# Performance work log

Hardware: AMD Instinct MI355X
Metric: run time of the kernel (lower is better)

Reference implementation:

```python
import jax, jax.numpy as jnp
import numpy as np
from jax import lax

VOCAB, EMB, HID = 50257, 256, 256
B, T = 64, 2048

def setup_inputs() -> dict:
    key = jax.random.key(0)
    ks = jax.random.split(key, 6)
    s = 1.0 / np.sqrt(HID)
    return {
        "sequence": jax.random.randint(ks[0], (B, T), 0, VOCAB),
        "embedding": jax.random.normal(ks[1], (VOCAB, EMB), jnp.float32),
        "w_ih": jax.random.uniform(ks[2], (3 * HID, EMB), jnp.float32, -s, s),
        "w_hh": jax.random.uniform(ks[3], (3 * HID, HID), jnp.float32, -s, s),
        "b_ih": jax.random.uniform(ks[4], (3 * HID,), jnp.float32, -s, s),
        "b_hh": jax.random.uniform(ks[5], (3 * HID,), jnp.float32, -s, s),
    }

def reference(sequence, embedding, w_ih, w_hh, b_ih, b_hh):
    # sequence: [B,T] int tokens. Original loops per-timestep; math == one GRU pass.
    H = w_hh.shape[1]
    x = embedding[sequence]                       # [B,T,E]
    x = jnp.transpose(x, (1, 0, 2))               # [T,B,E] (time-major)
    # input-side gate pre-activations for all steps at once: [T,B,3H]
    gi = jnp.einsum('tbe,ge->tbg', x, w_ih) + b_ih

    def step(h, gi_t):
        gh = h @ w_hh.T + b_hh                    # [B,3H]
        i_r, i_z, i_n = jnp.split(gi_t, 3, axis=-1)
        h_r, h_z, h_n = jnp.split(gh, 3, axis=-1)
        r = jax.nn.sigmoid(i_r + h_r)
        z = jax.nn.sigmoid(i_z + h_z)
        n = jnp.tanh(i_n + r * h_n)
        h_new = (1.0 - z) * n + z * h
        return h_new, None

    h0 = jnp.zeros((sequence.shape[0], H), dtype=embedding.dtype)
    hT, _ = lax.scan(step, h0, gi)
    return hT[None]                                # [1,B,H] like torch GRU hidden
```

## Files before the change

### kernel.cpp

```cpp
#include <hip/hip_runtime.h>
#include <hip/hip_fp16.h>

#define TSEQ   2048
#define NB     64
#define NE     256
#define NH     256
#define NG     768
#define TCH    64
#define NCHUNK (TSEQ / TCH)

using half2_t = __attribute__((ext_vector_type(2))) _Float16;
typedef unsigned int u32x4 __attribute__((ext_vector_type(4)));
union U4 { u32x4 q; half2_t h[4]; };

__device__ __forceinline__ float dot2f(half2_t a, half2_t b, float c) {
#if __has_builtin(__builtin_amdgcn_fdot2)
  return __builtin_amdgcn_fdot2(a, b, c, false);
#else
  return c + (float)a[0] * (float)b[0] + (float)a[1] * (float)b[1];
#endif
}

__device__ __forceinline__ float fast_exp2(float x) {
#if __has_builtin(__builtin_amdgcn_exp2f)
  return __builtin_amdgcn_exp2f(x);
#else
  return exp2f(x);
#endif
}
__device__ __forceinline__ float fast_rcp(float x) {
#if __has_builtin(__builtin_amdgcn_rcpf)
  return __builtin_amdgcn_rcpf(x);
#else
  return 1.f / x;
#endif
}
__device__ __forceinline__ float sigm(float x) {
  return fast_rcp(1.f + fast_exp2(x * -1.44269504f));
}
__device__ __forceinline__ float tanh_fast(float x) {
  x = fminf(x, 15.f);
  float e = fast_exp2(x * 2.88539008f);
  return (e - 1.f) * fast_rcp(e + 1.f);
}

__global__ void prep_whh(const float* __restrict__ whh, unsigned int* __restrict__ w16) {
  int idx = blockIdx.x * 256 + threadIdx.x;
  if (idx >= 128 * NG) return;
  int row = idx % NG;
  int k2  = idx / NG;
  half2_t p;
  p[0] = (_Float16)whh[row * NH + 2 * k2];
  p[1] = (_Float16)whh[row * NH + 2 * k2 + 1];
  union { half2_t h; unsigned int u; } cvt;
  cvt.h = p;
  w16[(((k2 >> 2) * NG + row) << 2) | (k2 & 3)] = cvt.u;
}

__global__ __launch_bounds__(1024)
void fused_kernel(const int* __restrict__ seq, const float* __restrict__ emb,
                  const float* __restrict__ wih, const float* __restrict__ bih,
                  const float* __restrict__ bhh, const unsigned int* __restrict__ w16,
                  const float* __restrict__ rec_gi, float* __restrict__ gi_dst,
                  int gi_t0, float* __restrict__ h_state, float* __restrict__ out,
                  int rec_count, int chunk)
{
  __shared__ __align__(16) char smem[87552];
  const int tid = threadIdx.x;

  if ((int)blockIdx.x < rec_count) {
    _Float16* h16 = (_Float16*)smem;
    const int b    = blockIdx.x;
    const int lane = tid & 63;
    const int wv   = tid >> 6;
    const int j    = wv * 16 + (lane & 15);
    const int s    = lane >> 4;

#define LOADW(i)                                                              \
  u32x4 wr##i, wz##i, wn##i;                                                  \
  {                                                                           \
    const unsigned int* base = w16 + (((size_t)(s * 8 + (i)) * NG) << 2);     \
    wr##i = *(const u32x4*)(base + ((size_t)j << 2));                         \
    wz##i = *(const u32x4*)(base + ((size_t)(NH + j) << 2));                  \
    wn##i = *(const u32x4*)(base + ((size_t)(2 * NH + j) << 2));              \
  }
    LOADW(0) LOADW(1) LOADW(2) LOADW(3) LOADW(4) LOADW(5) LOADW(6) LOADW(7)
#undef LOADW
    asm volatile("" : "+v"(wr0), "+v"(wr1), "+v"(wr2), "+v"(wr3),
                      "+v"(wr4), "+v"(wr5), "+v"(wr6), "+v"(wr7));
    asm volatile("" : "+v"(wz0), "+v"(wz1), "+v"(wz2), "+v"(wz3),
                      "+v"(wz4), "+v"(wz5), "+v"(wz6), "+v"(wz7));
    asm volatile("" : "+v"(wn0), "+v"(wn1), "+v"(wn2), "+v"(wn3),
                      "+v"(wn4), "+v"(wn5), "+v"(wn6), "+v"(wn7));

    const float bn = bhh[2 * NH + j];
    float hreg = 0.f;
    if (chunk != 0) hreg = h_state[b * NH + j];
    if (s == 0) h16[j] = (_Float16)hreg;
    __syncthreads();

    const float* gpj = rec_gi + (size_t)b * NG + j;

#pragma unroll 1
    for (int t = 0; t < TCH; ++t) {
      const float gr = gpj[0], gz = gpj[NH], gn = gpj[2 * NH];

      float ar = 0.f, az = 0.f, an = 0.f;
      const char* hb = (const char*)h16 + ((t & 1) << 9) + (s << 7);

#define DOT(i)                                                                \
  {                                                                           \
    U4 hu; hu.q = *(const u32x4*)(hb + ((i) << 4));                           \
    U4 ru; ru.q = wr##i;                                                      \
    U4 zu; zu.q = wz##i;                                                      \
    U4 nu; nu.q = wn##i;                                                      \
    ar = dot2f(hu.h[0], ru.h[0], ar);                                         \
    az = dot2f(hu.h[0], zu.h[0], az);                                         \
    an = dot2f(hu.h[0], nu.h[0], an);                                         \
    ar = dot2f(hu.h[1], ru.h[1], ar);                                         \
    az = dot2f(hu.h[1], zu.h[1], az);                                         \
    an = dot2f(hu.h[1], nu.h[1], an);                                         \
    ar = dot2f(hu.h[2], ru.h[2], ar);                                         \
    az = dot2f(hu.h[2], zu.h[2], az);                                         \
    an = dot2f(hu.h[2], nu.h[2], an);                                         \
    ar = dot2f(hu.h[3], ru.h[3], ar);                                         \
    az = dot2f(hu.h[3], zu.h[3], az);                                         \
    an = dot2f(hu.h[3], nu.h[3], an);                                         \
  }
      DOT(0) DOT(1) DOT(2) DOT(3) DOT(4) DOT(5) DOT(6) DOT(7)
#undef DOT

      ar += __shfl_xor(ar, 16, 64);  ar += __shfl_xor(ar, 32, 64);
      az += __shfl_xor(az, 16, 64);  az += __shfl_xor(az, 32, 64);
      an += __shfl_xor(an, 16, 64);  an += __shfl_xor(an, 32, 64);

      const float r = sigm(gr + ar);
      const float z = sigm(gz + az);
      const float n = tanh_fast(gn + r * (an + bn));
      hreg = n + z * (hreg - n);

      if (s == 0) h16[(((t + 1) & 1) << 8) + j] = (_Float16)hreg;
      gpj += NB * NG;
      __syncthreads();
    }
    if (s == 0) {
      h_state[b * NH + j] = hreg;
      if (out) out[b * NH + j] = hreg;
    }
  } else {
    if (gi_dst == nullptr) return;
    float (*xs)[68]  = (float(*)[68])smem;
    float (*wsh)[68] = (float(*)[68])(smem + 17408);
    int*  tok        = (int*)(smem + 17408 + 69632);
    const int gb = blockIdx.x - rec_count;
    const int tl = gb & 63;
    const int g0 = (gb >> 6) * 256;
    const int t  = gi_t0 + tl;
    if (tid < 64) tok[tid] = seq[tid * TSEQ + t];
    const int tx = tid & 31;
    const int ty = tid >> 5;
    float acc[2][8];
#pragma unroll
    for (int i = 0; i < 2; ++i)
#pragma unroll
      for (int c8 = 0; c8 < 8; ++c8) acc[i][c8] = 0.f;

    for (int kb = 0; kb < 4; ++kb) {
      __syncthreads();
      {
        int r = tid >> 4, c = tid & 15;
        *(float4*)(&xs[r][c * 4]) =
            *(const float4*)(emb + (size_t)tok[r] * NE + kb * 64 + c * 4);
      }
#pragma unroll
      for (int it = 0; it < 4; ++it) {
        int i = it * 1024 + tid;
        int r = i >> 4, c = i & 15;
        *(float4*)(&wsh[r][c * 4]) =
            *(const float4*)(wih + (size_t)(g0 + r) * NE + kb * 64 + c * 4);
      }
      __syncthreads();
#pragma unroll 4
      for (int k4 = 0; k4 < 16; ++k4) {
        float4 xf[2], wf[8];
#pragma unroll
        for (int i = 0; i < 2; ++i) xf[i] = *(const float4*)(&xs[ty * 2 + i][k4 * 4]);
#pragma unroll
        for (int c8 = 0; c8 < 8; ++c8) wf[c8] = *(const float4*)(&wsh[tx + 32 * c8][k4 * 4]);
#pragma unroll
        for (int i = 0; i < 2; ++i)
#pragma unroll
          for (int c8 = 0; c8 < 8; ++c8)
            acc[i][c8] += xf[i].x * wf[c8].x + xf[i].y * wf[c8].y +
                          xf[i].z * wf[c8].z + xf[i].w * wf[c8].w;
      }
    }
#pragma unroll
    for (int i = 0; i < 2; ++i) {
      const int brow = ty * 2 + i;
      float* dst = gi_dst + ((size_t)(tl * NB + brow)) * NG + g0;
#pragma unroll
      for (int c8 = 0; c8 < 8; ++c8) {
        const int col = tx + 32 * c8;
        const int g = g0 + col;
        float bias = bih[g] + (g < 2 * NH ? bhh[g] : 0.f);
        dst[col] = acc[i][c8] + bias;
      }
    }
  }
}

extern "C" void kernel_launch(void* const* d_in, const int* in_sizes, int n_in,
                              void* d_out, int out_size, void* d_ws, size_t ws_size,
                              hipStream_t stream) {
  (void)in_sizes; (void)n_in; (void)out_size; (void)ws_size;
  const int*   seq = (const int*)d_in[0];
  const float* emb = (const float*)d_in[1];
  const float* wih = (const float*)d_in[2];
  const float* whh = (const float*)d_in[3];
  const float* bih = (const float*)d_in[4];
  const float* bhh = (const float*)d_in[5];
  float* out = (float*)d_out;
  char*  ws  = (char*)d_ws;

  unsigned int* w16     = (unsigned int*)(ws);
  float*        h_state = (float*)(ws + 393216);
  float*        gi0     = (float*)(ws + 458752);
  float*        gi1     = (float*)(ws + 458752 + 12582912);

  prep_whh<<<dim3(384), dim3(256), 0, stream>>>(whh, w16);

  fused_kernel<<<dim3(192), dim3(1024), 0, stream>>>(
      seq, emb, wih, bih, bhh, w16,
      nullptr, gi0, 0, h_state, nullptr, 0, 0);

  for (int c = 0; c < NCHUNK; ++c) {
    float* rd  = (c & 1) ? gi1 : gi0;
    float* wr_ = (c & 1) ? gi0 : gi1;
    const bool last = (c == NCHUNK - 1);
    const int grid  = last ? NB : NB + 192;
    fused_kernel<<<dim3(grid), dim3(1024), 0, stream>>>(
        seq, emb, wih, bih, bhh, w16,
        rd, last ? nullptr : wr_, (c + 1) * TCH, h_state,
        last ? out : nullptr, NB, c);
  }
}
```

Measured before the change: 2.674 ms.

## Move n-gate recurrent weights from registers into LDS and pad h buffer

The n-gate W_hh slice is repacked by a new prep kernel into a per-lane LDS image and loaded into shared memory at block start, so the recurrent loop keeps only the r and z weights in VGPRs. This cuts register pressure (32 fewer u32x4 registers per thread), which could allow better scheduling or avoid spills. The h double-buffer is also re-laid out with padded quarter strides to reduce LDS bank conflicts. The cost is an extra LDS read per dot step inside the serial loop and a larger shared allocation of about 129 KB.

```diff
diff --git a/kernel.cpp b/kernel.cpp
--- a/kernel.cpp
+++ b/kernel.cpp
@@ -8,6 +8,12 @@
 #define NG     768
 #define TCH    64
 #define NCHUNK (TSEQ / TCH)
+
+#define WN_BYTES   131072
+#define H_OFF      131072
+#define H_BUFSTR   576
+#define H_QSTR     144
+#define POOL_BYTES 132352
 
 using half2_t = __attribute__((ext_vector_type(2))) _Float16;
 typedef unsigned int u32x4 __attribute__((ext_vector_type(4)));
@@ -57,32 +63,62 @@
   w16[(((k2 >> 2) * NG + row) << 2) | (k2 & 3)] = cvt.u;
 }
 
+__global__ void prep_n(const float* __restrict__ whh, unsigned int* __restrict__ n_img) {
+  int idx32 = blockIdx.x * 256 + threadIdx.x;
+  if (idx32 >= 32768) return;
+  int idxh = idx32 * 2;
+  int wv   = idxh >> 12;
+  int r    = idxh & 4095;
+  int i    = r >> 9;
+  int r2   = r & 511;
+  int lane = r2 >> 3;
+  int e    = r2 & 7;
+  int j    = wv * 16 + (lane & 15);
+  int s    = lane >> 4;
+  int k    = s * 64 + i * 8 + e;
+  half2_t p;
+  p[0] = (_Float16)whh[(512 + j) * NH + k];
+  p[1] = (_Float16)whh[(512 + j) * NH + k + 1];
+  union { half2_t h; unsigned int u; } cvt;
+  cvt.h = p;
+  n_img[idx32] = cvt.u;
+}
+
 __global__ __launch_bounds__(1024)
 void fused_kernel(const int* __restrict__ seq, const float* __restrict__ emb,
                   const float* __restrict__ wih, const float* __restrict__ bih,
                   const float* __restrict__ bhh, const unsigned int* __restrict__ w16,
+                  const unsigned int* __restrict__ n_img,
                   const float* __restrict__ rec_gi, float* __restrict__ gi_dst,
                   int gi_t0, float* __restrict__ h_state, float* __restrict__ out,
                   int rec_count, int chunk)
 {
-  __shared__ __align__(16) char smem[87552];
+  __shared__ __align__(16) char smem[POOL_BYTES];
   const int tid = threadIdx.x;
 
   if ((int)blockIdx.x < rec_count) {
-    _Float16* h16 = (_Float16*)smem;
     const int b    = blockIdx.x;
     const int lane = tid & 63;
     const int wv   = tid >> 6;
     const int j    = wv * 16 + (lane & 15);
     const int s    = lane >> 4;
 
+    {
+      const char* nsrc = (const char*)n_img;
+      const int base = wv * 8192 + lane * 16;
+#pragma unroll
+      for (int it = 0; it < 8; ++it) {
+        *(u32x4*)(smem + base + it * 1024) =
+            *(const u32x4*)(nsrc + base + it * 1024);
+      }
+    }
+
 #define LOADW(i)                                                              \
-  u32x4 wr##i, wz##i, wn##i;                                                  \
+  u32x4 wr##i, wz##i;                                                         \
   {                                                                           \
     const unsigned int* base = w16 + (((size_t)(s * 8 + (i)) * NG) << 2);     \
     wr##i = *(const u32x4*)(base + ((size_t)j << 2));                         \
     wz##i = *(const u32x4*)(base + ((size_t)(NH + j) << 2));                  \
-    wn##i = *(const u32x4*)(base + ((size_t)(2 * NH + j) << 2));              \
   }
     LOADW(0) LOADW(1) LOADW(2) LOADW(3) LOADW(4) LOADW(5) LOADW(6) LOADW(7)
 #undef LOADW
@@ -90,30 +126,32 @@
                       "+v"(wr4), "+v"(wr5), "+v"(wr6), "+v"(wr7));
     asm volatile("" : "+v"(wz0), "+v"(wz1), "+v"(wz2), "+v"(wz3),
                       "+v"(wz4), "+v"(wz5), "+v"(wz6), "+v"(wz7));
-    asm volatile("" : "+v"(wn0), "+v"(wn1), "+v"(wn2), "+v"(wn3),
-                      "+v"(wn4), "+v"(wn5), "+v"(wn6), "+v"(wn7));
 
     const float bn = bhh[2 * NH + j];
     float hreg = 0.f;
     if (chunk != 0) hreg = h_state[b * NH + j];
-    if (s == 0) h16[j] = (_Float16)hreg;
+    if (s == 0) {
+      *(_Float16*)(smem + H_OFF + ((j >> 6) * H_QSTR) + ((j & 63) * 2)) =
+          (_Float16)hreg;
+    }
     __syncthreads();
 
     const float* gpj = rec_gi + (size_t)b * NG + j;
+    const char*  nb  = smem + wv * 8192 + lane * 16;
 
 #pragma unroll 1
     for (int t = 0; t < TCH; ++t) {
       const float gr = gpj[0], gz = gpj[NH], gn = gpj[2 * NH];
 
       float ar = 0.f, az = 0.f, an = 0.f;
-      const char* hb = (const char*)h16 + ((t & 1) << 9) + (s << 7);
+      const char* hb = smem + H_OFF + ((t & 1) ? H_BUFSTR : 0) + s * H_QSTR;
 
 #define DOT(i)                                                                \
   {                                                                           \
     U4 hu; hu.q = *(const u32x4*)(hb + ((i) << 4));                           \
+    U4 nu; nu.q = *(const u32x4*)(nb + ((i) << 10));                          \
     U4 ru; ru.q = wr##i;                                                      \
     U4 zu; zu.q = wz##i;                                                      \
-    U4 nu; nu.q = wn##i;                                                      \
     ar = dot2f(hu.h[0], ru.h[0], ar);                                         \
     az = dot2f(hu.h[0], zu.h[0], az);                                         \
     an = dot2f(hu.h[0], nu.h[0], an);                                         \
@@ -139,7 +177,10 @@
       const float n = tanh_fast(gn + r * (an + bn));
       hreg = n + z * (hreg - n);
 
-      if (s == 0) h16[(((t + 1) & 1) << 8) + j] = (_Float16)hreg;
+      if (s == 0) {
+        *(_Float16*)(smem + H_OFF + (((t + 1) & 1) ? H_BUFSTR : 0) +
+                     ((j >> 6) * H_QSTR) + ((j & 63) * 2)) = (_Float16)hreg;
+      }
       gpj += NB * NG;
       __syncthreads();
     }
@@ -224,14 +265,16 @@
   char*  ws  = (char*)d_ws;
 
   unsigned int* w16     = (unsigned int*)(ws);
-  float*        h_state = (float*)(ws + 393216);
-  float*        gi0     = (float*)(ws + 458752);
-  float*        gi1     = (float*)(ws + 458752 + 12582912);
+  unsigned int* n_img   = (unsigned int*)(ws + 393216);
+  float*        h_state = (float*)(ws + 524288);
+  float*        gi0     = (float*)(ws + 589824);
+  float*        gi1     = (float*)(ws + 589824 + 12582912);
 
   prep_whh<<<dim3(384), dim3(256), 0, stream>>>(whh, w16);
+  prep_n  <<<dim3(128), dim3(256), 0, stream>>>(whh, n_img);
 
   fused_kernel<<<dim3(192), dim3(1024), 0, stream>>>(
-      seq, emb, wih, bih, bhh, w16,
+      seq, emb, wih, bih, bhh, w16, n_img,
       nullptr, gi0, 0, h_state, nullptr, 0, 0);
 
   for (int c = 0; c < NCHUNK; ++c) {
@@ -240,7 +283,7 @@
     const bool last = (c == NCHUNK - 1);
     const int grid  = last ? NB : NB + 192;
     fused_kernel<<<dim3(grid), dim3(1024), 0, stream>>>(
-        seq, emb, wih, bih, bhh, w16,
+        seq, emb, wih, bih, bhh, w16, n_img,
         rd, last ? nullptr : wr_, (c + 1) * TCH, h_state,
         last ? out : nullptr, NB, c);
   }
```

Result: slower. 2.770 ms (+3.6%).
